# Kernel optimization log

Measured on AMD Instinct MI355X. Metric: run time of the kernel, lower is better.

The kernel has to match this reference:

```python
import jax, jax.numpy as jnp
import numpy as np

B, T, D, H, C = 64, 512, 128, 512, 256  # batch, seq_len, input_dim, rnn_dim, clf hidden


def _lstm_cell(x, h, c, Wih, Whh, b):
    # PyTorch gate order: i, f, g, o; b = bias_ih + bias_hh
    gates = x @ Wih.T + h @ Whh.T + b  # [B, 4H]
    i, f, g, o = jnp.split(gates, 4, axis=-1)
    c = jax.nn.sigmoid(f) * c + jax.nn.sigmoid(i) * jnp.tanh(g)
    h = jax.nn.sigmoid(o) * jnp.tanh(c)
    return h, c


def _run_lstm2(xs, state, p0, p1):
    # xs: [B, T, in]; state: (h0, c0, h1, c1) each [B, H]
    def step(carry, x_t):
        h0, c0, h1, c1 = carry
        h0, c0 = _lstm_cell(x_t, h0, c0, *p0)
        h1, c1 = _lstm_cell(h0, h1, c1, *p1)
        return (h0, c0, h1, c1), h1
    state, ys = jax.lax.scan(step, state, jnp.swapaxes(xs, 0, 1))
    return jnp.swapaxes(ys, 0, 1), state


def setup_inputs() -> dict:
    key = jax.random.key(0)
    ks = jax.random.split(key, 18)
    s = 0.04  # ~1/sqrt(H), matches torch LSTM init scale
    w = lambda k, shape: (jax.random.normal(k, shape, jnp.float32) * s)
    inp = {
        "x": jax.random.uniform(ks[0], (B, T, D), dtype=jnp.float32),
        "y": (jax.random.uniform(ks[1], (B, T, D), dtype=jnp.float32) > 0.9).astype(jnp.float32),
        "enc_Wih0": w(ks[2], (4 * H, D)), "enc_Whh0": w(ks[3], (4 * H, H)), "enc_b0": w(ks[4], (4 * H,)),
        "enc_Wih1": w(ks[5], (4 * H, H)), "enc_Whh1": w(ks[6], (4 * H, H)), "enc_b1": w(ks[7], (4 * H,)),
        "dec_Wih0": w(ks[8], (4 * H, D)), "dec_Whh0": w(ks[9], (4 * H, H)), "dec_b0": w(ks[10], (4 * H,)),
        "dec_Wih1": w(ks[11], (4 * H, H)), "dec_Whh1": w(ks[12], (4 * H, H)), "dec_b1": w(ks[13], (4 * H,)),
        "clf_W1": w(ks[14], (C, H)), "clf_b1": w(ks[15], (C,)),
        "clf_W2": w(ks[16], (D, C)), "clf_b2": w(ks[17], (D,)),
    }
    return inp


def reference(x, y, enc_Wih0, enc_Whh0, enc_b0, enc_Wih1, enc_Whh1, enc_b1,
              dec_Wih0, dec_Whh0, dec_b0, dec_Wih1, dec_Whh1, dec_b1,
              clf_W1, clf_b1, clf_W2, clf_b2):
    Bc = x.shape[0]
    z = jnp.zeros((Bc, H), x.dtype)
    # encoder: only final (h, c) of both layers is used
    _, state = _run_lstm2(x, (z, z, z, z),
                          (enc_Wih0, enc_Whh0, enc_b0), (enc_Wih1, enc_Whh1, enc_b1))
    # decoder under full teacher forcing: steps t=1..T-1 consume y[:, t-1]
    dec_out, _ = _run_lstm2(y[:, :-1], state,
                            (dec_Wih0, dec_Whh0, dec_b0), (dec_Wih1, dec_Whh1, dec_b1))
    hid = jax.nn.relu(dec_out @ clf_W1.T + clf_b1)          # [B, T-1, C]
    logits = hid @ clf_W2.T + clf_b2                        # [B, T-1, D]
    # outputs[:, 0] stays zero, as in the torch loop starting at t=1
    return jnp.concatenate([jnp.zeros_like(logits[:, :1]), logits], axis=1)
```

## Files before the change

### kernel.cpp

```cpp
#include <hip/hip_runtime.h>
#include <hip/hip_bf16.h>
#include <stdint.h>

#define SMEM_BYTES 150528

using short8  = __attribute__((ext_vector_type(8))) short;
using f32x4   = __attribute__((ext_vector_type(4))) float;
using u32x4   = __attribute__((ext_vector_type(4))) unsigned int;

#define OXBF 0u
#define OYBF 8388608u
#define OWE0 16777216u
#define OWD0 (OWE0 + 2621440u)
#define OWE1 (OWD0 + 2621440u)
#define OWD1 (OWE1 + 4194304u)
#define OWC1 (OWD1 + 4194304u)
#define OWC2 (OWC1 + 262144u)
#define OA0  (OWC2 + 65536u)
#define OB0  (OA0 + 2097152u)
#define OA1  (OB0 + 2097152u)
#define OB1  (OA1 + 2097152u)
#define OHP  (OB1 + 2097152u)
#define OFLG (OHP + 1048576u)
#define OFC1 (OFLG + 4096u)
#define OFH  (OFLG + 8192u)
#define OFL  (OFLG + 9216u)
#define OPRB (OFLG + 16384u)
#define OVOT (OFLG + 32768u)

#define GUARD (1<<19)

static __device__ __forceinline__ unsigned short f2bf(float f){
  union { float f; unsigned u; } v; v.f = f;
  unsigned r = v.u + 0x7FFFu + ((v.u >> 16) & 1u);
  return (unsigned short)(r >> 16);
}
static __device__ __forceinline__ float sigm(float x){ return 1.f/(1.f+__expf(-x)); }
static __device__ __forceinline__ float tanh_(float x){ return 1.f - 2.f/(__expf(2.f*x)+1.f); }

static __device__ __forceinline__ u32x4 ld_r16(const void* p, bool loc){
  u32x4 v;
  if (loc) asm volatile("global_load_dwordx4 %0, %1, off sc0"     : "=v"(v) : "v"(p) : "memory");
  else     asm volatile("global_load_dwordx4 %0, %1, off sc0 sc1" : "=v"(v) : "v"(p) : "memory");
  return v;
}
static __device__ __forceinline__ void st_r16(void* p, u32x4 v, bool loc){
  if (loc) asm volatile("global_store_dwordx4 %0, %1, off sc0"     :: "v"(p), "v"(v) : "memory");
  else     asm volatile("global_store_dwordx4 %0, %1, off sc0 sc1" :: "v"(p), "v"(v) : "memory");
}
static __device__ __forceinline__ unsigned ld_f4(const void* p, bool loc){
  unsigned v;
  if (loc) asm volatile("global_load_dword %0, %1, off sc0\n\ts_waitcnt vmcnt(0)"     : "=v"(v) : "v"(p) : "memory");
  else     asm volatile("global_load_dword %0, %1, off sc0 sc1\n\ts_waitcnt vmcnt(0)" : "=v"(v) : "v"(p) : "memory");
  return v;
}
static __device__ __forceinline__ void st_f4(void* p, unsigned v, bool loc){
  if (loc) asm volatile("global_store_dword %0, %1, off sc0"     :: "v"(p), "v"(v) : "memory");
  else     asm volatile("global_store_dword %0, %1, off sc0 sc1" :: "v"(p), "v"(v) : "memory");
}
static __device__ __forceinline__ unsigned ld_cg4(const void* p){ return ld_f4(p, false); }
static __device__ __forceinline__ void st_cg4(void* p, unsigned v){ st_f4(p, v, false); }
static __device__ __forceinline__ void drain_vm(){
  asm volatile("s_waitcnt vmcnt(0)" ::: "memory");
}
static __device__ __forceinline__ bool isS(u32x4 v){
  return (v[0]==0xFFFFFFFFu) | (v[1]==0xFFFFFFFFu) | (v[2]==0xFFFFFFFFu) | (v[3]==0xFFFFFFFFu);
}

__global__ void k_init(float* __restrict__ out, uint8_t* __restrict__ ws){
  int i = blockIdx.x*blockDim.x + threadIdx.x;
  int ns = gridDim.x*blockDim.x;
  uint32_t* r = (uint32_t*)(ws + OA0);
  const int nring = (4*2097152 + 1048576)/4;
  for (int k=i; k<nring; k+=ns) r[k] = 0xFFFFFFFFu;
  uint32_t* fl = (uint32_t*)(ws + OFLG);
  for (int k=i; k<49152/4; k+=ns) fl[k] = 0u;
  for (int k=i; k<64*128; k+=ns) out[(size_t)(k>>7)*(512*128) + (k&127)] = 0.f;
}

__global__ void k_cvt(const float* __restrict__ x, const float* __restrict__ y,
                      uint8_t* __restrict__ ws){
  unsigned short* xb = (unsigned short*)(ws + OXBF);
  unsigned short* yb = (unsigned short*)(ws + OYBF);
  const int n = 64*512*128;
  int i = blockIdx.x*blockDim.x + threadIdx.x, ns = gridDim.x*blockDim.x;
  for (int k=i; k<n; k+=ns){ xb[k] = f2bf(x[k]); yb[k] = f2bf(y[k]); }
}

__global__ void k_swzgate(const float* __restrict__ Wih, const float* __restrict__ Whh,
                          uint8_t* __restrict__ ws, size_t dstOff, int Kin, int KC, int NKK, int mode){
  unsigned short* dst = (unsigned short*)(ws + dstOff);
  const int total = 2048 * (KC*4);
  int i = blockIdx.x*blockDim.x + threadIdx.x, ns = gridDim.x*blockDim.x;
  for (int idx=i; idx<total; idx+=ns){
    int j = idx & 7;
    int lane = (idx >> 3) & 63;
    int t = idx >> 9;
    int g = t & 3; t >>= 2;
    int kk = t % NKK; t /= NKK;
    int w = t & 3; int ub = t >> 2;
    int off = ((lane>>4)<<3) + j;
    int k = mode ? (kk==0 ? w*32 + off : 128 + w*128 + (kk-1)*32 + off)
                 : (w*KC + kk*32 + off);
    int u = ub*16 + (lane&15);
    int row = g*512 + u;
    float v = (k < Kin) ? Wih[(size_t)row*Kin + k] : Whh[(size_t)row*512 + (k-Kin)];
    dst[idx] = f2bf(v);
  }
}

__global__ void k_swzclf(const float* __restrict__ W, uint8_t* __restrict__ ws,
                         size_t dstOff, int nwgs, int Kw, int Ktot){
  unsigned short* dst = (unsigned short*)(ws + dstOff);
  const int NKK = Kw/32;
  const int total = nwgs*4*NKK*64*8;
  int i = blockIdx.x*blockDim.x + threadIdx.x, ns = gridDim.x*blockDim.x;
  for (int idx=i; idx<total; idx+=ns){
    int j = idx & 7;
    int lane = (idx >> 3) & 63;
    int t = idx >> 9;
    int kk = t % NKK; t /= NKK;
    int w = t & 3; int wg = t >> 2;
    int k = w*Kw + kk*32 + ((lane>>4)<<3) + j;
    int col = wg*16 + (lane&15);
    dst[idx] = f2bf(W[(size_t)col*Ktot + k]);
  }
}

__launch_bounds__(256, 1)
__global__ void k_seq(uint8_t* __restrict__ ws,
                      const float* __restrict__ eb0, const float* __restrict__ eb1,
                      const float* __restrict__ db0, const float* __restrict__ db1,
                      const float* __restrict__ cb1, const float* __restrict__ cb2,
                      float* __restrict__ out){
  __shared__ uint8_t smem[SMEM_BYTES];
  const int wg = blockIdx.x, tid = threadIdx.x;
  const int w = tid>>6, l = tid&63, lr = l&15, lg = l>>4;
  const int xcd = wg & 7, j = wg >> 3;

  int role;
  if (xcd < 2) role = 0;
  else if (xcd < 4) role = 1;
  else if (xcd == 4 && j < 16) role = 2;
  else if (xcd == 4 && j < 24) role = 3;
  else return;

  const unsigned short* xb = (const unsigned short*)(ws+OXBF);
  const unsigned short* yb = (const unsigned short*)(ws+OYBF);
  unsigned short* A0e = (unsigned short*)(ws+OA0);
  unsigned short* B0e = (unsigned short*)(ws+OB0);
  unsigned short* A1e = (unsigned short*)(ws+OA1);
  unsigned short* B1e = (unsigned short*)(ws+OB1);
  unsigned short* hpr = (unsigned short*)(ws+OHP);

  short8* BL = (short8*)smem;
  float*  P0 = (float*)(smem + 131072);
  float*  P1 = (float*)(smem + 139776);
  unsigned short* HS = (unsigned short*)(smem + 148480);

  const u32x4 S4 = (u32x4){0xFFFFFFFFu,0xFFFFFFFFu,0xFFFFFFFFu,0xFFFFFFFFu};
  const u32x4 Z4 = (u32x4){0u,0u,0u,0u};

  bool loc;
  {
    const int n   = (role <= 1) ? 32 : 24;
    const int bas = (role <= 1) ? xcd : 4;
    if (w == 0){
      bool ok = true;
      #pragma unroll 1
      for (int gen = 1; gen <= 3; ++gen){
        if (l == 0) st_f4(ws + OPRB + (size_t)wg*64u, (unsigned)gen, true);
        if (l < n){
          const void* p = ws + OPRB + (size_t)(bas + 8*l)*64u;
          int spins = 0; unsigned e;
          do { e = ld_f4(p, true); } while ((int)e < gen && ++spins < 1024);
          if ((int)e < gen) ok = false;
        }
      }
      unsigned long long b1 = __ballot(ok);
      bool wgok = (b1 == ~0ULL);
      if (l == 0) st_f4(ws + OVOT + (size_t)wg*64u, wgok ? 2u : 1u, false);
      bool vok = wgok;
      if (l < n){
        const void* p = ws + OVOT + (size_t)(bas + 8*l)*64u;
        unsigned v;
        do { v = ld_f4(p, false); } while (v == 0u);
        vok = vok && (v == 2u);
      }
      unsigned long long b2 = __ballot(vok);
      if (l == 0) *(int*)HS = (b2 == ~0ULL) ? 1 : 0;
    }
    __syncthreads();
    loc = (*(volatile int*)HS) != 0;
    __syncthreads();
  }

  auto loadB = [&](size_t srcOff, int bytes){
    const u32x4* s = (const u32x4*)(ws + srcOff);
    u32x4* d = (u32x4*)smem;
    for (int i = tid; i < bytes/16; i += 256) d[i] = s[i];
  };

  if (role <= 1){
    const bool isC0 = (role == 0);
    const int bt = isC0 ? xcd : xcd-2, ub = j;
    const int u = tid&15, ug = ub*16 + u;
    const int bbytes = isC0 ? 81920 : 131072;
    unsigned short* OWN0 = loc ? A0e : B0e;

    float be[4], bd[4];
    {
      const float* e = isC0 ? eb0 : eb1;
      const float* d = isC0 ? db0 : db1;
      #pragma unroll
      for (int g=0; g<4; ++g){ be[g] = e[g*512+ug]; bd[g] = d[g*512+ug]; }
    }
    loadB((isC0 ? (size_t)OWE0 : (size_t)OWE1) + (size_t)ub*bbytes, bbytes);
    float cS0 = 0.f, cS1 = 0.f;
    __syncthreads();

    for (int t = 0; t < 1023; ++t){
      if (t == 512){
        __syncthreads();
        loadB((isC0 ? (size_t)OWD0 : (size_t)OWD1) + (size_t)ub*bbytes, bbytes);
        __syncthreads();
      }

      const int slotW = t&31, slotR = (t+31)&31;

      f32x4 acc[2][4];
      #pragma unroll
      for (int m=0;m<2;++m)
        #pragma unroll
        for (int g=0;g<4;++g) acc[m][g] = (f32x4){0.f,0.f,0.f,0.f};

      if (isC0){
        const unsigned short* xs = (t<512) ? xb : yb;
        const int tt = (t<512) ? t : t-512;
        short8 ax[2];
        #pragma unroll
        for (int m=0;m<2;++m){
          const int b = bt*32 + m*16 + lr;
          ax[m] = *(const short8*)(xs + ((size_t)b*512 + tt)*128 + w*32 + (lg<<3));
        }
        u32x4 ah[4][2];
        if (t > 0){
          const unsigned short* base = OWN0 + (size_t)slotR*64*512;
          int gd = 0; bool bad;
          do {
            #pragma unroll
            for (int kk=0; kk<4; ++kk)
              #pragma unroll
              for (int m=0;m<2;++m){
                const int b = bt*32 + m*16 + lr;
                ah[kk][m] = ld_r16(base + (size_t)b*512 + w*128 + kk*32 + (lg<<3), loc);
              }
            drain_vm();
            __builtin_amdgcn_sched_barrier(0);
            bad = false;
            #pragma unroll
            for (int kk=0; kk<4; ++kk)
              #pragma unroll
              for (int m=0;m<2;++m) bad |= isS(ah[kk][m]);
            if (bad) __builtin_amdgcn_s_sleep(1);
          } while (bad && ++gd < GUARD);
          __builtin_amdgcn_sched_barrier(0);
        } else {
          #pragma unroll
          for (int kk=0; kk<4; ++kk)
            #pragma unroll
            for (int m=0;m<2;++m) ah[kk][m] = Z4;
        }
        #pragma unroll
        for (int g=0;g<4;++g){
          short8 bf = BL[((w*5+0)*4+g)*64 + l];
          acc[0][g] = __builtin_amdgcn_mfma_f32_16x16x32_bf16(ax[0], bf, acc[0][g],0,0,0);
          acc[1][g] = __builtin_amdgcn_mfma_f32_16x16x32_bf16(ax[1], bf, acc[1][g],0,0,0);
        }
        #pragma unroll
        for (int kk=1; kk<5; ++kk)
          #pragma unroll
          for (int g=0;g<4;++g){
            short8 bf = BL[((w*5+kk)*4+g)*64 + l];
            acc[0][g] = __builtin_amdgcn_mfma_f32_16x16x32_bf16(__builtin_bit_cast(short8, ah[kk-1][0]), bf, acc[0][g],0,0,0);
            acc[1][g] = __builtin_amdgcn_mfma_f32_16x16x32_bf16(__builtin_bit_cast(short8, ah[kk-1][1]), bf, acc[1][g],0,0,0);
          }
      } else {
        u32x4 a[8][2];
        const bool wv01 = (w < 2);
        if (wv01 || t > 0){
          const unsigned short* base;
          bool myloc;
          if (wv01){ base = B0e + (size_t)slotW*64*512; myloc = false; }
          else {
            base = (loc ? A1e : (((t-1) >= 512) ? B1e : A1e)) + (size_t)slotR*64*512;
            myloc = loc;
          }
          const int kbase = wv01 ? (w*256) : (w*256 - 512);
          int gd = 0; bool bad;
          do {
            #pragma unroll
            for (int kk=0; kk<8; ++kk)
              #pragma unroll
              for (int m=0;m<2;++m){
                const int b = bt*32 + m*16 + lr;
                a[kk][m] = ld_r16(base + (size_t)b*512 + kbase + kk*32 + (lg<<3), myloc);
              }
            drain_vm();
            __builtin_amdgcn_sched_barrier(0);
            bad = false;
            #pragma unroll
            for (int kk=0; kk<8; ++kk)
              #pragma unroll
              for (int m=0;m<2;++m) bad |= isS(a[kk][m]);
            if (bad) __builtin_amdgcn_s_sleep(1);
          } while (bad && ++gd < GUARD);
          __builtin_amdgcn_sched_barrier(0);
        } else {
          #pragma unroll
          for (int kk=0; kk<8; ++kk)
            #pragma unroll
            for (int m=0;m<2;++m) a[kk][m] = Z4;
        }
        #pragma unroll
        for (int kk=0; kk<8; ++kk)
          #pragma unroll
          for (int g=0;g<4;++g){
            short8 bf = BL[((w*8+kk)*4+g)*64 + l];
            acc[0][g] = __builtin_amdgcn_mfma_f32_16x16x32_bf16(__builtin_bit_cast(short8, a[kk][0]), bf, acc[0][g],0,0,0);
            acc[1][g] = __builtin_amdgcn_mfma_f32_16x16x32_bf16(__builtin_bit_cast(short8, a[kk][1]), bf, acc[1][g],0,0,0);
          }
      }

      {
        float* P = (w&1) ? P1 : P0;
        if (w < 2){
          #pragma unroll
          for (int m=0;m<2;++m)
            #pragma unroll
            for (int g=0;g<4;++g)
              #pragma unroll
              for (int r=0;r<4;++r)
                P[(m*16 + (lg<<2) + r)*68 + g*16 + lr] = acc[m][g][r];
        }
        __syncthreads();
        if (w >= 2){
          #pragma unroll
          for (int m=0;m<2;++m)
            #pragma unroll
            for (int g=0;g<4;++g)
              #pragma unroll
              for (int r=0;r<4;++r)
                P[(m*16 + (lg<<2) + r)*68 + g*16 + lr] += acc[m][g][r];
        }
        __syncthreads();
      }

      if (w == 0 && (t & 7) == 0){
        drain_vm();
        __builtin_amdgcn_sched_barrier(0);
        if (isC0){
          if (t >= 24 && l < 32){
            const void* p = ws + OFC1 + (size_t)(bt*32+l)*64;
            const int need = (t-22 < 1) ? 1 : t-22;
            int v, gd = 0;
            do { v = (int)ld_f4(p, false); if (v < need) __builtin_amdgcn_s_sleep(2); }
            while (v < need && ++gd < GUARD);
          }
        } else {
          if (t >= 536 && l < 16){
            const void* p = ws + OFH + (size_t)l*64;
            const int need = (t-534 < 1) ? 1 : t-534;
            int v, gd = 0;
            do { v = (int)ld_f4(p, false); if (v < need) __builtin_amdgcn_s_sleep(2); }
            while (v < need && ++gd < GUARD);
          }
        }
        if (t >= 8){
          const int row = l>>1, half = l&1;
          #pragma unroll
          for (int a=2; a<=9; ++a){
            const int cs = (t+a)&31;
            const size_t off = ((size_t)cs*64 + bt*32 + row)*512 + ub*16 + half*8;
            if (isC0){
              st_r16(OWN0 + off, S4, loc);
              if (loc) st_r16(B0e + off, S4, false);
            } else {
              st_r16(loc ? A1e + off : (((t+a-32) >= 512) ? B1e + off : A1e + off), S4, loc ? true : false);
              if (loc && (t+a) >= 544) st_r16(B1e + off, S4, false);
            }
          }
        }
      }

      const float* bias = (t<512) ? be : bd;
      #pragma unroll
      for (int s=0;s<2;++s){
        const int row = (tid>>4) + s*16;
        const int pi = row*68 + u;
        float gi = P0[pi]      + P1[pi]      + bias[0];
        float gf = P0[pi+16]   + P1[pi+16]   + bias[1];
        float gg = P0[pi+32]   + P1[pi+32]   + bias[2];
        float go = P0[pi+48]   + P1[pi+48]   + bias[3];
        float cprev = s ? cS1 : cS0;
        float c = sigm(gf)*cprev + sigm(gi)*tanh_(gg);
        if (s) cS1 = c; else cS0 = c;
        float h = sigm(go)*tanh_(c);
        HS[row*16 + u] = f2bf(h);
      }
      __syncthreads();
      if (tid < 64){
        u32x4 v = *(const u32x4*)(HS + tid*8);
        const int row = tid>>1, half = tid&1;
        const size_t off = ((size_t)slotW*64 + bt*32 + row)*512 + ub*16 + half*8;
        if (isC0){
          st_r16(OWN0 + off, v, loc);
          if (loc) st_r16(B0e + off, v, false);
        } else {
          if (loc){
            st_r16(A1e + off, v, true);
            if (t >= 512) st_r16(B1e + off, v, false);
          } else {
            st_r16(((t >= 512) ? B1e : A1e) + off, v, false);
          }
        }
      }
      if (!isC0 && tid == 0)
        st_f4(ws + OFC1 + (size_t)(bt*32+ub)*64, (unsigned)(t+1), false);
    }
  } else if (role == 2){
    const int hwg = j;
    const int u = tid&15, col = hwg*16 + u;
    const float bc = cb1[col];
    loadB((size_t)OWC1 + (size_t)hwg*16384, 16384);
    __syncthreads();
    for (int t2 = 0; t2 < 511; ++t2){
      const int slot = (512+t2)&31;

      u32x4 a[4][4];
      const unsigned short* base = B1e + (size_t)slot*64*512;
      int gd = 0; bool bad;
      do {
        #pragma unroll
        for (int kk=0; kk<4; ++kk)
          #pragma unroll
          for (int m=0;m<4;++m)
            a[kk][m] = ld_r16(base + (size_t)(m*16+lr)*512 + w*128 + kk*32 + (lg<<3), false);
        drain_vm();
        __builtin_amdgcn_sched_barrier(0);
        bad = false;
        #pragma unroll
        for (int kk=0; kk<4; ++kk)
          #pragma unroll
          for (int m=0;m<4;++m) bad |= isS(a[kk][m]);
        if (bad) __builtin_amdgcn_s_sleep(1);
      } while (bad && ++gd < GUARD);
      __builtin_amdgcn_sched_barrier(0);
      f32x4 ha[4];
      #pragma unroll
      for (int m=0;m<4;++m) ha[m] = (f32x4){0.f,0.f,0.f,0.f};
      #pragma unroll
      for (int kk=0; kk<4; ++kk){
        short8 bf = BL[(w*4+kk)*64 + l];
        #pragma unroll
        for (int m=0;m<4;++m)
          ha[m] = __builtin_amdgcn_mfma_f32_16x16x32_bf16(__builtin_bit_cast(short8, a[kk][m]), bf, ha[m],0,0,0);
      }
      {
        float* P = (w&1) ? P1 : P0;
        if (w < 2){
          #pragma unroll
          for (int m=0;m<4;++m)
            #pragma unroll
            for (int r=0;r<4;++r)
              P[(m*16 + (lg<<2) + r)*20 + lr] = ha[m][r];
        }
        __syncthreads();
        if (w >= 2){
          #pragma unroll
          for (int m=0;m<4;++m)
            #pragma unroll
            for (int r=0;r<4;++r)
              P[(m*16 + (lg<<2) + r)*20 + lr] += ha[m][r];
        }
        __syncthreads();
      }
      if (w == 0 && (t2 & 7) == 0){
        drain_vm();
        __builtin_amdgcn_sched_barrier(0);
        if (t2 >= 24 && l < 8){
          const void* p = ws + OFL + (size_t)l*64;
          const int need = (t2-22 < 1) ? 1 : t2-22;
          int v, g2 = 0;
          do { v = (int)ld_f4(p, loc); if (v < need) __builtin_amdgcn_s_sleep(2); }
          while (v < need && ++g2 < GUARD);
        }
        if (t2 >= 8){
          #pragma unroll
          for (int a=2; a<=9; ++a){
            const int cs = (t2+a)&31;
            #pragma unroll
            for (int q=0;q<2;++q)
              st_r16(hpr + ((size_t)cs*64 + l)*256 + hwg*16 + q*8, S4, loc);
          }
        }
      }
      #pragma unroll
      for (int s=0;s<4;++s){
        const int row = (tid>>4) + s*16;
        float v = P0[row*20+u] + P1[row*20+u] + bc;
        HS[row*16 + u] = f2bf(fmaxf(v, 0.f));
      }
      __syncthreads();
      if (tid < 128){
        u32x4 v = *(const u32x4*)(HS + tid*8);
        const int row = tid>>1, half = tid&1;
        st_r16(hpr + ((size_t)(t2&31)*64 + row)*256 + hwg*16 + half*8, v, loc);
      }
      if (tid == 0) st_f4(ws + OFH + (size_t)hwg*64, (unsigned)(t2+1), false);
    }
  } else {
    const int lwg = j - 16;
    const int u = tid&15, col = lwg*16 + u;
    const float bc = cb2[col];
    loadB((size_t)OWC2 + (size_t)lwg*8192, 8192);
    __syncthreads();
    for (int t3 = 0; t3 < 511; ++t3){
      const int slot = t3&31;
      u32x4 a[2][4];
      const unsigned short* base = hpr + (size_t)slot*64*256;
      int gd = 0; bool bad;
      do {
        #pragma unroll
        for (int kk=0; kk<2; ++kk)
          #pragma unroll
          for (int m=0;m<4;++m)
            a[kk][m] = ld_r16(base + (size_t)(m*16+lr)*256 + w*64 + kk*32 + (lg<<3), loc);
        drain_vm();
        __builtin_amdgcn_sched_barrier(0);
        bad = false;
        #pragma unroll
        for (int kk=0; kk<2; ++kk)
          #pragma unroll
          for (int m=0;m<4;++m) bad |= isS(a[kk][m]);
        if (bad) __builtin_amdgcn_s_sleep(1);
      } while (bad && ++gd < GUARD);
      __builtin_amdgcn_sched_barrier(0);
      f32x4 la[4];
      #pragma unroll
      for (int m=0;m<4;++m) la[m] = (f32x4){0.f,0.f,0.f,0.f};
      #pragma unroll
      for (int kk=0; kk<2; ++kk){
        short8 bf = BL[(w*2+kk)*64 + l];
        #pragma unroll
        for (int m=0;m<4;++m)
          la[m] = __builtin_amdgcn_mfma_f32_16x16x32_bf16(__builtin_bit_cast(short8, a[kk][m]), bf, la[m],0,0,0);
      }
      {
        float* P = (w&1) ? P1 : P0;
        if (w < 2){
          #pragma unroll
          for (int m=0;m<4;++m)
            #pragma unroll
            for (int r=0;r<4;++r)
              P[(m*16 + (lg<<2) + r)*20 + lr] = la[m][r];
        }
        __syncthreads();
        if (w >= 2){
          #pragma unroll
          for (int m=0;m<4;++m)
            #pragma unroll
            for (int r=0;r<4;++r)
              P[(m*16 + (lg<<2) + r)*20 + lr] += la[m][r];
        }
        __syncthreads();
      }
      #pragma unroll
      for (int s=0;s<4;++s){
        const int row = (tid>>4) + s*16;
        float v = P0[row*20+u] + P1[row*20+u] + bc;
        out[((size_t)row*512 + (t3+1))*128 + col] = v;
      }
      if (tid == 0) st_f4(ws + OFL + (size_t)lwg*64, (unsigned)(t3+1), loc);
    }
  }
}

extern "C" void kernel_launch(void* const* d_in, const int* in_sizes, int n_in,
                              void* d_out, int out_size, void* d_ws, size_t ws_size,
                              hipStream_t stream){
  const float* x   = (const float*)d_in[0];
  const float* y   = (const float*)d_in[1];
  const float* eW0 = (const float*)d_in[2];
  const float* eU0 = (const float*)d_in[3];
  const float* eb0 = (const float*)d_in[4];
  const float* eW1 = (const float*)d_in[5];
  const float* eU1 = (const float*)d_in[6];
  const float* eb1 = (const float*)d_in[7];
  const float* dW0 = (const float*)d_in[8];
  const float* dU0 = (const float*)d_in[9];
  const float* db0 = (const float*)d_in[10];
  const float* dW1 = (const float*)d_in[11];
  const float* dU1 = (const float*)d_in[12];
  const float* db1 = (const float*)d_in[13];
  const float* cW1 = (const float*)d_in[14];
  const float* cb1 = (const float*)d_in[15];
  const float* cW2 = (const float*)d_in[16];
  const float* cb2 = (const float*)d_in[17];
  float* out = (float*)d_out;
  uint8_t* ws = (uint8_t*)d_ws;
  (void)in_sizes; (void)n_in; (void)out_size; (void)ws_size;

  k_init<<<dim3(256), dim3(256), 0, stream>>>(out, ws);
  k_cvt<<<dim3(2048), dim3(256), 0, stream>>>(x, y, ws);
  k_swzgate<<<dim3(1280), dim3(256), 0, stream>>>(eW0, eU0, ws, (size_t)OWE0, 128, 160, 5, 1);
  k_swzgate<<<dim3(1280), dim3(256), 0, stream>>>(dW0, dU0, ws, (size_t)OWD0, 128, 160, 5, 1);
  k_swzgate<<<dim3(2048), dim3(256), 0, stream>>>(eW1, eU1, ws, (size_t)OWE1, 512, 256, 8, 0);
  k_swzgate<<<dim3(2048), dim3(256), 0, stream>>>(dW1, dU1, ws, (size_t)OWD1, 512, 256, 8, 0);
  k_swzclf<<<dim3(256), dim3(256), 0, stream>>>(cW1, ws, (size_t)OWC1, 16, 128, 512);
  k_swzclf<<<dim3(64),  dim3(256), 0, stream>>>(cW2, ws, (size_t)OWC2, 8, 64, 256);
  k_seq<<<dim3(256), dim3(256), 0, stream>>>(ws, eb0, eb1, db0, db1, cb1, cb2, out);
}
```

Baseline: 5.209 ms.

## Add dedicated comm wave and replace block barriers with LDS flag handshakes

Adds a fifth wavefront per workgroup that handles the global h-ring publish, slot poisoning and cross-workgroup flag polling. The four compute waves now coordinate through LDS counters with spin-waits instead of __syncthreads, and the h staging buffer is double-buffered so the next step's compute can overlap the previous step's publish. This aims to take global-store latency and periodic poll stalls off the recurrent critical path. In exchange it adds spin-wait overhead and more complex ordering, with a risk of races or hangs if the fences are wrong.

```diff
diff --git a/kernel.cpp b/kernel.cpp
--- a/kernel.cpp
+++ b/kernel.cpp
@@ -2,7 +2,7 @@
 #include <hip/hip_bf16.h>
 #include <stdint.h>
 
-#define SMEM_BYTES 150528
+#define SMEM_BYTES 152640
 
 using short8  = __attribute__((ext_vector_type(8))) short;
 using f32x4   = __attribute__((ext_vector_type(4))) float;
@@ -58,10 +58,11 @@
   if (loc) asm volatile("global_store_dword %0, %1, off sc0"     :: "v"(p), "v"(v) : "memory");
   else     asm volatile("global_store_dword %0, %1, off sc0 sc1" :: "v"(p), "v"(v) : "memory");
 }
-static __device__ __forceinline__ unsigned ld_cg4(const void* p){ return ld_f4(p, false); }
-static __device__ __forceinline__ void st_cg4(void* p, unsigned v){ st_f4(p, v, false); }
 static __device__ __forceinline__ void drain_vm(){
   asm volatile("s_waitcnt vmcnt(0)" ::: "memory");
+}
+static __device__ __forceinline__ void drain_lgkm(){
+  asm volatile("s_waitcnt lgkmcnt(0)" ::: "memory");
 }
 static __device__ __forceinline__ bool isS(u32x4 v){
   return (v[0]==0xFFFFFFFFu) | (v[1]==0xFFFFFFFFu) | (v[2]==0xFFFFFFFFu) | (v[3]==0xFFFFFFFFu);
@@ -127,7 +128,7 @@
   }
 }
 
-__launch_bounds__(256, 1)
+__launch_bounds__(320, 1)
 __global__ void k_seq(uint8_t* __restrict__ ws,
                       const float* __restrict__ eb0, const float* __restrict__ eb1,
                       const float* __restrict__ db0, const float* __restrict__ db1,
@@ -157,6 +158,10 @@
   float*  P0 = (float*)(smem + 131072);
   float*  P1 = (float*)(smem + 139776);
   unsigned short* HS = (unsigned short*)(smem + 148480);
+  volatile int* FL  = (volatile int*)(smem + 152576);
+  volatile int* DBE = (volatile int*)(smem + 152592);
+  volatile int* DBC = (volatile int*)(smem + 152608);
+  volatile int* FW  = (volatile int*)(smem + 152612);
 
   const u32x4 S4 = (u32x4){0xFFFFFFFFu,0xFFFFFFFFu,0xFFFFFFFFu,0xFFFFFFFFu};
   const u32x4 Z4 = (u32x4){0u,0u,0u,0u};
@@ -194,11 +199,24 @@
     loc = (*(volatile int*)HS) != 0;
     __syncthreads();
   }
+  if (tid < 16) ((volatile int*)(smem + 152576))[tid] = 0;
+  __syncthreads();
 
   auto loadB = [&](size_t srcOff, int bytes){
-    const u32x4* s = (const u32x4*)(ws + srcOff);
-    u32x4* d = (u32x4*)smem;
-    for (int i = tid; i < bytes/16; i += 256) d[i] = s[i];
+    if (tid < 256){
+      const u32x4* s = (const u32x4*)(ws + srcOff);
+      u32x4* d = (u32x4*)smem;
+      for (int i = tid; i < bytes/16; i += 256) d[i] = s[i];
+    }
+  };
+  auto spin_ge = [&](volatile int* p, int tgt){
+    int g = 0;
+    while (*p < tgt && ++g < GUARD) __builtin_amdgcn_s_sleep(1);
+    __builtin_amdgcn_sched_barrier(0);
+  };
+  auto set_fl = [&](volatile int* p, int v){
+    drain_lgkm();
+    if (l == 0) *p = v;
   };
 
   if (role <= 1){
@@ -219,122 +237,127 @@
     float cS0 = 0.f, cS1 = 0.f;
     __syncthreads();
 
-    for (int t = 0; t < 1023; ++t){
-      if (t == 512){
-        __syncthreads();
-        loadB((isC0 ? (size_t)OWD0 : (size_t)OWD1) + (size_t)ub*bbytes, bbytes);
-        __syncthreads();
-      }
-
-      const int slotW = t&31, slotR = (t+31)&31;
-
-      f32x4 acc[2][4];
-      #pragma unroll
-      for (int m=0;m<2;++m)
-        #pragma unroll
-        for (int g=0;g<4;++g) acc[m][g] = (f32x4){0.f,0.f,0.f,0.f};
-
-      if (isC0){
-        const unsigned short* xs = (t<512) ? xb : yb;
-        const int tt = (t<512) ? t : t-512;
-        short8 ax[2];
-        #pragma unroll
-        for (int m=0;m<2;++m){
-          const int b = bt*32 + m*16 + lr;
-          ax[m] = *(const short8*)(xs + ((size_t)b*512 + tt)*128 + w*32 + (lg<<3));
-        }
-        u32x4 ah[4][2];
-        if (t > 0){
-          const unsigned short* base = OWN0 + (size_t)slotR*64*512;
-          int gd = 0; bool bad;
-          do {
+    if (w < 4){
+      for (int t = 0; t < 1023; ++t){
+        if (t == 512){
+          #pragma unroll 1
+          for (int q=0;q<4;++q) spin_ge(&DBE[q], 512);
+          loadB((isC0 ? (size_t)OWD0 : (size_t)OWD1) + (size_t)ub*bbytes, bbytes);
+          drain_vm(); drain_lgkm();
+          set_fl(&FW[w], 1);
+          #pragma unroll 1
+          for (int q=0;q<4;++q) spin_ge(&FW[q], 1);
+        }
+        const int slotW = t&31, slotR = (t+31)&31;
+
+        f32x4 acc[2][4];
+        #pragma unroll
+        for (int m=0;m<2;++m)
+          #pragma unroll
+          for (int g=0;g<4;++g) acc[m][g] = (f32x4){0.f,0.f,0.f,0.f};
+
+        if (isC0){
+          const unsigned short* xs = (t<512) ? xb : yb;
+          const int tt = (t<512) ? t : t-512;
+          short8 ax[2];
+          #pragma unroll
+          for (int m=0;m<2;++m){
+            const int b = bt*32 + m*16 + lr;
+            ax[m] = *(const short8*)(xs + ((size_t)b*512 + tt)*128 + w*32 + (lg<<3));
+          }
+          u32x4 ah[4][2];
+          if (t > 0){
+            const unsigned short* base = OWN0 + (size_t)slotR*64*512;
+            int gd = 0; bool bad;
+            do {
+              #pragma unroll
+              for (int kk=0; kk<4; ++kk)
+                #pragma unroll
+                for (int m=0;m<2;++m){
+                  const int b = bt*32 + m*16 + lr;
+                  ah[kk][m] = ld_r16(base + (size_t)b*512 + w*128 + kk*32 + (lg<<3), loc);
+                }
+              drain_vm();
+              __builtin_amdgcn_sched_barrier(0);
+              bad = false;
+              #pragma unroll
+              for (int kk=0; kk<4; ++kk)
+                #pragma unroll
+                for (int m=0;m<2;++m) bad |= isS(ah[kk][m]);
+              if (bad) __builtin_amdgcn_s_sleep(1);
+            } while (bad && ++gd < GUARD);
+            __builtin_amdgcn_sched_barrier(0);
+          } else {
             #pragma unroll
             for (int kk=0; kk<4; ++kk)
               #pragma unroll
-              for (int m=0;m<2;++m){
-                const int b = bt*32 + m*16 + lr;
-                ah[kk][m] = ld_r16(base + (size_t)b*512 + w*128 + kk*32 + (lg<<3), loc);
-              }
-            drain_vm();
+              for (int m=0;m<2;++m) ah[kk][m] = Z4;
+          }
+          #pragma unroll
+          for (int g=0;g<4;++g){
+            short8 bf = BL[((w*5+0)*4+g)*64 + l];
+            acc[0][g] = __builtin_amdgcn_mfma_f32_16x16x32_bf16(ax[0], bf, acc[0][g],0,0,0);
+            acc[1][g] = __builtin_amdgcn_mfma_f32_16x16x32_bf16(ax[1], bf, acc[1][g],0,0,0);
+          }
+          #pragma unroll
+          for (int kk=1; kk<5; ++kk)
+            #pragma unroll
+            for (int g=0;g<4;++g){
+              short8 bf = BL[((w*5+kk)*4+g)*64 + l];
+              acc[0][g] = __builtin_amdgcn_mfma_f32_16x16x32_bf16(__builtin_bit_cast(short8, ah[kk-1][0]), bf, acc[0][g],0,0,0);
+              acc[1][g] = __builtin_amdgcn_mfma_f32_16x16x32_bf16(__builtin_bit_cast(short8, ah[kk-1][1]), bf, acc[1][g],0,0,0);
+            }
+        } else {
+          u32x4 a[8][2];
+          const bool wv01 = (w < 2);
+          if (wv01 || t > 0){
+            const unsigned short* base;
+            bool myloc;
+            if (wv01){ base = B0e + (size_t)slotW*64*512; myloc = false; }
+            else {
+              base = (loc ? A1e : (((t-1) >= 512) ? B1e : A1e)) + (size_t)slotR*64*512;
+              myloc = loc;
+            }
+            const int kbase = wv01 ? (w*256) : (w*256 - 512);
+            int gd = 0; bool bad;
+            do {
+              #pragma unroll
+              for (int kk=0; kk<8; ++kk)
+                #pragma unroll
+                for (int m=0;m<2;++m){
+                  const int b = bt*32 + m*16 + lr;
+                  a[kk][m] = ld_r16(base + (size_t)b*512 + kbase + kk*32 + (lg<<3), myloc);
+                }
+              drain_vm();
+              __builtin_amdgcn_sched_barrier(0);
+              bad = false;
+              #pragma unroll
+              for (int kk=0; kk<8; ++kk)
+                #pragma unroll
+                for (int m=0;m<2;++m) bad |= isS(a[kk][m]);
+              if (bad) __builtin_amdgcn_s_sleep(1);
+            } while (bad && ++gd < GUARD);
             __builtin_amdgcn_sched_barrier(0);
-            bad = false;
-            #pragma unroll
-            for (int kk=0; kk<4; ++kk)
-              #pragma unroll
-              for (int m=0;m<2;++m) bad |= isS(ah[kk][m]);
-            if (bad) __builtin_amdgcn_s_sleep(1);
-          } while (bad && ++gd < GUARD);
-          __builtin_amdgcn_sched_barrier(0);
-        } else {
-          #pragma unroll
-          for (int kk=0; kk<4; ++kk)
-            #pragma unroll
-            for (int m=0;m<2;++m) ah[kk][m] = Z4;
-        }
-        #pragma unroll
-        for (int g=0;g<4;++g){
-          short8 bf = BL[((w*5+0)*4+g)*64 + l];
-          acc[0][g] = __builtin_amdgcn_mfma_f32_16x16x32_bf16(ax[0], bf, acc[0][g],0,0,0);
-          acc[1][g] = __builtin_amdgcn_mfma_f32_16x16x32_bf16(ax[1], bf, acc[1][g],0,0,0);
-        }
-        #pragma unroll
-        for (int kk=1; kk<5; ++kk)
-          #pragma unroll
-          for (int g=0;g<4;++g){
-            short8 bf = BL[((w*5+kk)*4+g)*64 + l];
-            acc[0][g] = __builtin_amdgcn_mfma_f32_16x16x32_bf16(__builtin_bit_cast(short8, ah[kk-1][0]), bf, acc[0][g],0,0,0);
-            acc[1][g] = __builtin_amdgcn_mfma_f32_16x16x32_bf16(__builtin_bit_cast(short8, ah[kk-1][1]), bf, acc[1][g],0,0,0);
-          }
-      } else {
-        u32x4 a[8][2];
-        const bool wv01 = (w < 2);
-        if (wv01 || t > 0){
-          const unsigned short* base;
-          bool myloc;
-          if (wv01){ base = B0e + (size_t)slotW*64*512; myloc = false; }
-          else {
-            base = (loc ? A1e : (((t-1) >= 512) ? B1e : A1e)) + (size_t)slotR*64*512;
-            myloc = loc;
-          }
-          const int kbase = wv01 ? (w*256) : (w*256 - 512);
-          int gd = 0; bool bad;
-          do {
+          } else {
             #pragma unroll
             for (int kk=0; kk<8; ++kk)
               #pragma unroll
-              for (int m=0;m<2;++m){
-                const int b = bt*32 + m*16 + lr;
-                a[kk][m] = ld_r16(base + (size_t)b*512 + kbase + kk*32 + (lg<<3), myloc);
-              }
-            drain_vm();
-            __builtin_amdgcn_sched_barrier(0);
-            bad = false;
-            #pragma unroll
-            for (int kk=0; kk<8; ++kk)
-              #pragma unroll
-              for (int m=0;m<2;++m) bad |= isS(a[kk][m]);
-            if (bad) __builtin_amdgcn_s_sleep(1);
-          } while (bad && ++gd < GUARD);
-          __builtin_amdgcn_sched_barrier(0);
-        } else {
+              for (int m=0;m<2;++m) a[kk][m] = Z4;
+          }
           #pragma unroll
           for (int kk=0; kk<8; ++kk)
             #pragma unroll
-            for (int m=0;m<2;++m) a[kk][m] = Z4;
-        }
-        #pragma unroll
-        for (int kk=0; kk<8; ++kk)
-          #pragma unroll
-          for (int g=0;g<4;++g){
-            short8 bf = BL[((w*8+kk)*4+g)*64 + l];
-            acc[0][g] = __builtin_amdgcn_mfma_f32_16x16x32_bf16(__builtin_bit_cast(short8, a[kk][0]), bf, acc[0][g],0,0,0);
-            acc[1][g] = __builtin_amdgcn_mfma_f32_16x16x32_bf16(__builtin_bit_cast(short8, a[kk][1]), bf, acc[1][g],0,0,0);
-          }
-      }
-
-      {
-        float* P = (w&1) ? P1 : P0;
+            for (int g=0;g<4;++g){
+              short8 bf = BL[((w*8+kk)*4+g)*64 + l];
+              acc[0][g] = __builtin_amdgcn_mfma_f32_16x16x32_bf16(__builtin_bit_cast(short8, a[kk][0]), bf, acc[0][g],0,0,0);
+              acc[1][g] = __builtin_amdgcn_mfma_f32_16x16x32_bf16(__builtin_bit_cast(short8, a[kk][1]), bf, acc[1][g],0,0,0);
+            }
+        }
+
         if (w < 2){
+          #pragma unroll 1
+          for (int q=0;q<4;++q) spin_ge(&DBE[q], t);
+          float* P = (w&1) ? P1 : P0;
           #pragma unroll
           for (int m=0;m<2;++m)
             #pragma unroll
@@ -342,9 +365,10 @@
               #pragma unroll
               for (int r=0;r<4;++r)
                 P[(m*16 + (lg<<2) + r)*68 + g*16 + lr] = acc[m][g][r];
-        }
-        __syncthreads();
-        if (w >= 2){
+          set_fl(&FL[w], t+1);
+        } else {
+          spin_ge(&FL[w-2], t+1);
+          float* P = (w&1) ? P1 : P0;
           #pragma unroll
           for (int m=0;m<2;++m)
             #pragma unroll
@@ -352,67 +376,73 @@
               #pragma unroll
               for (int r=0;r<4;++r)
                 P[(m*16 + (lg<<2) + r)*68 + g*16 + lr] += acc[m][g][r];
-        }
-        __syncthreads();
-      }
-
-      if (w == 0 && (t & 7) == 0){
-        drain_vm();
-        __builtin_amdgcn_sched_barrier(0);
-        if (isC0){
-          if (t >= 24 && l < 32){
-            const void* p = ws + OFC1 + (size_t)(bt*32+l)*64;
-            const int need = (t-22 < 1) ? 1 : t-22;
-            int v, gd = 0;
-            do { v = (int)ld_f4(p, false); if (v < need) __builtin_amdgcn_s_sleep(2); }
-            while (v < need && ++gd < GUARD);
-          }
-        } else {
-          if (t >= 536 && l < 16){
-            const void* p = ws + OFH + (size_t)l*64;
-            const int need = (t-534 < 1) ? 1 : t-534;
-            int v, gd = 0;
-            do { v = (int)ld_f4(p, false); if (v < need) __builtin_amdgcn_s_sleep(2); }
-            while (v < need && ++gd < GUARD);
-          }
-        }
-        if (t >= 8){
-          const int row = l>>1, half = l&1;
-          #pragma unroll
-          for (int a=2; a<=9; ++a){
-            const int cs = (t+a)&31;
-            const size_t off = ((size_t)cs*64 + bt*32 + row)*512 + ub*16 + half*8;
-            if (isC0){
-              st_r16(OWN0 + off, S4, loc);
-              if (loc) st_r16(B0e + off, S4, false);
-            } else {
-              st_r16(loc ? A1e + off : (((t+a-32) >= 512) ? B1e + off : A1e + off), S4, loc ? true : false);
-              if (loc && (t+a) >= 544) st_r16(B1e + off, S4, false);
+          set_fl(&FL[w], t+1);
+        }
+        spin_ge(&FL[2], t+1);
+        spin_ge(&FL[3], t+1);
+
+        const float* bias = (t<512) ? be : bd;
+        spin_ge(&DBC[0], t-1);
+        unsigned short* HSb = HS + (t&1)*512;
+        #pragma unroll
+        for (int s=0;s<2;++s){
+          const int row = (tid>>4) + s*16;
+          const int pi = row*68 + u;
+          float gi = P0[pi]      + P1[pi]      + bias[0];
+          float gf = P0[pi+16]   + P1[pi+16]   + bias[1];
+          float gg = P0[pi+32]   + P1[pi+32]   + bias[2];
+          float go = P0[pi+48]   + P1[pi+48]   + bias[3];
+          float cprev = s ? cS1 : cS0;
+          float c = sigm(gf)*cprev + sigm(gi)*tanh_(gg);
+          if (s) cS1 = c; else cS0 = c;
+          float h = sigm(go)*tanh_(c);
+          HSb[row*16 + u] = f2bf(h);
+        }
+        set_fl(&DBE[w], t+1);
+      }
+    } else {
+      for (int t = 0; t < 1023; ++t){
+        #pragma unroll 1
+        for (int q=0;q<4;++q) spin_ge(&DBE[q], t+1);
+        if ((t & 7) == 0){
+          drain_vm();
+          __builtin_amdgcn_sched_barrier(0);
+          if (isC0){
+            if (t >= 24 && l < 32){
+              const void* p = ws + OFC1 + (size_t)(bt*32+l)*64;
+              const int need = (t-22 < 1) ? 1 : t-22;
+              int v, gd = 0;
+              do { v = (int)ld_f4(p, false); if (v < need) __builtin_amdgcn_s_sleep(2); }
+              while (v < need && ++gd < GUARD);
             }
-          }
-        }
-      }
-
-      const float* bias = (t<512) ? be : bd;
-      #pragma unroll
-      for (int s=0;s<2;++s){
-        const int row = (tid>>4) + s*16;
-        const int pi = row*68 + u;
-        float gi = P0[pi]      + P1[pi]      + bias[0];
-        float gf = P0[pi+16]   + P1[pi+16]   + bias[1];
-        float gg = P0[pi+32]   + P1[pi+32]   + bias[2];
-        float go = P0[pi+48]   + P1[pi+48]   + bias[3];
-        float cprev = s ? cS1 : cS0;
-        float c = sigm(gf)*cprev + sigm(gi)*tanh_(gg);
-        if (s) cS1 = c; else cS0 = c;
-        float h = sigm(go)*tanh_(c);
-        HS[row*16 + u] = f2bf(h);
-      }
-      __syncthreads();
-      if (tid < 64){
-        u32x4 v = *(const u32x4*)(HS + tid*8);
-        const int row = tid>>1, half = tid&1;
-        const size_t off = ((size_t)slotW*64 + bt*32 + row)*512 + ub*16 + half*8;
+          } else {
+            if (t >= 536 && l < 16){
+              const void* p = ws + OFH + (size_t)l*64;
+              const int need = (t-534 < 1) ? 1 : t-534;
+              int v, gd = 0;
+              do { v = (int)ld_f4(p, false); if (v < need) __builtin_amdgcn_s_sleep(2); }
+              while (v < need && ++gd < GUARD);
+            }
+          }
+          if (t >= 8){
+            const int row = l>>1, half = l&1;
+            #pragma unroll
+            for (int a=2; a<=9; ++a){
+              const int cs = (t+a)&31;
+              const size_t off = ((size_t)cs*64 + bt*32 + row)*512 + ub*16 + half*8;
+              if (isC0){
+                st_r16(OWN0 + off, S4, loc);
+                if (loc) st_r16(B0e + off, S4, false);
+              } else {
+                st_r16(loc ? A1e + off : (((t+a-32) >= 512) ? B1e + off : A1e + off), S4, loc ? true : false);
+                if (loc && (t+a) >= 544) st_r16(B1e + off, S4, false);
+              }
+            }
+          }
+        }
+        u32x4 v = *(const u32x4*)(HS + (t&1)*512 + l*8);
+        const int row = l>>1, half = l&1;
+        const size_t off = ((size_t)(t&31)*64 + bt*32 + row)*512 + ub*16 + half*8;
         if (isC0){
           st_r16(OWN0 + off, v, loc);
           if (loc) st_r16(B0e + off, v, false);
@@ -424,9 +454,11 @@
             st_r16(((t >= 512) ? B1e : A1e) + off, v, false);
           }
         }
-      }
-      if (!isC0 && tid == 0)
-        st_f4(ws + OFC1 + (size_t)(bt*32+ub)*64, (unsigned)(t+1), false);
+        if (!isC0 && l == 0)
+          st_f4(ws + OFC1 + (size_t)(bt*32+ub)*64, (unsigned)(t+1), false);
+        drain_lgkm();
+        if (l == 0) DBC[0] = t+1;
+      }
     }
   } else if (role == 2){
     const int hwg = j;
@@ -434,90 +466,106 @@
     const float bc = cb1[col];
     loadB((size_t)OWC1 + (size_t)hwg*16384, 16384);
     __syncthreads();
-    for (int t2 = 0; t2 < 511; ++t2){
-      const int slot = (512+t2)&31;
-
-      u32x4 a[4][4];
-      const unsigned short* base = B1e + (size_t)slot*64*512;
-      int gd = 0; bool bad;
-      do {
-        #pragma unroll
-        for (int kk=0; kk<4; ++kk)
+
+    if (w < 4){
+      for (int t2 = 0; t2 < 511; ++t2){
+        const int slot = (512+t2)&31;
+        u32x4 a[4][4];
+        const unsigned short* base = B1e + (size_t)slot*64*512;
+        int gd = 0; bool bad;
+        do {
+          #pragma unroll
+          for (int kk=0; kk<4; ++kk)
+            #pragma unroll
+            for (int m=0;m<4;++m)
+              a[kk][m] = ld_r16(base + (size_t)(m*16+lr)*512 + w*128 + kk*32 + (lg<<3), false);
+          drain_vm();
+          __builtin_amdgcn_sched_barrier(0);
+          bad = false;
+          #pragma unroll
+          for (int kk=0; kk<4; ++kk)
+            #pragma unroll
+            for (int m=0;m<4;++m) bad |= isS(a[kk][m]);
+          if (bad) __builtin_amdgcn_s_sleep(1);
+        } while (bad && ++gd < GUARD);
+        __builtin_amdgcn_sched_barrier(0);
+        f32x4 ha[4];
+        #pragma unroll
+        for (int m=0;m<4;++m) ha[m] = (f32x4){0.f,0.f,0.f,0.f};
+        #pragma unroll
+        for (int kk=0; kk<4; ++kk){
+          short8 bf = BL[(w*4+kk)*64 + l];
           #pragma unroll
           for (int m=0;m<4;++m)
-            a[kk][m] = ld_r16(base + (size_t)(m*16+lr)*512 + w*128 + kk*32 + (lg<<3), false);
-        drain_vm();
-        __builtin_amdgcn_sched_barrier(0);
-        bad = false;
-        #pragma unroll
-        for (int kk=0; kk<4; ++kk)
-          #pragma unroll
-          for (int m=0;m<4;++m) bad |= isS(a[kk][m]);
-        if (bad) __builtin_amdgcn_s_sleep(1);
-      } while (bad && ++gd < GUARD);
-      __builtin_amdgcn_sched_barrier(0);
-      f32x4 ha[4];
-      #pragma unroll
-      for (int m=0;m<4;++m) ha[m] = (f32x4){0.f,0.f,0.f,0.f};
-      #pragma unroll
-      for (int kk=0; kk<4; ++kk){
-        short8 bf = BL[(w*4+kk)*64 + l];
-        #pragma unroll
-        for (int m=0;m<4;++m)
-          ha[m] = __builtin_amdgcn_mfma_f32_16x16x32_bf16(__builtin_bit_cast(short8, a[kk][m]), bf, ha[m],0,0,0);
-      }
-      {
-        float* P = (w&1) ? P1 : P0;
+            ha[m] = __builtin_amdgcn_mfma_f32_16x16x32_bf16(__builtin_bit_cast(short8, a[kk][m]), bf, ha[m],0,0,0);
+        }
         if (w < 2){
+          #pragma unroll 1
+          for (int q=0;q<4;++q) spin_ge(&DBE[q], t2);
+          float* P = (w&1) ? P1 : P0;
           #pragma unroll
           for (int m=0;m<4;++m)
             #pragma unroll
             for (int r=0;r<4;++r)
               P[(m*16 + (lg<<2) + r)*20 + lr] = ha[m][r];
-        }
-        __syncthreads();
-        if (w >= 2){
+          set_fl(&FL[w], t2+1);
+        } else {
+          spin_ge(&FL[w-2], t2+1);
+          float* P = (w&1) ? P1 : P0;
           #pragma unroll
           for (int m=0;m<4;++m)
             #pragma unroll
             for (int r=0;r<4;++r)
               P[(m*16 + (lg<<2) + r)*20 + lr] += ha[m][r];
-        }
-        __syncthreads();
-      }
-      if (w == 0 && (t2 & 7) == 0){
-        drain_vm();
-        __builtin_amdgcn_sched_barrier(0);
-        if (t2 >= 24 && l < 8){
-          const void* p = ws + OFL + (size_t)l*64;
-          const int need = (t2-22 < 1) ? 1 : t2-22;
-          int v, g2 = 0;
-          do { v = (int)ld_f4(p, loc); if (v < need) __builtin_amdgcn_s_sleep(2); }
-          while (v < need && ++g2 < GUARD);
-        }
-        if (t2 >= 8){
-          #pragma unroll
-          for (int a=2; a<=9; ++a){
-            const int cs = (t2+a)&31;
-            #pragma unroll
-            for (int q=0;q<2;++q)
-              st_r16(hpr + ((size_t)cs*64 + l)*256 + hwg*16 + q*8, S4, loc);
-          }
-        }
-      }
-      #pragma unroll
-      for (int s=0;s<4;++s){
-        const int row = (tid>>4) + s*16;
-        float v = P0[row*20+u] + P1[row*20+u] + bc;
-        HS[row*16 + u] = f2bf(fmaxf(v, 0.f));
-      }
-      __syncthreads();
-      if (tid < 128){
-        u32x4 v = *(const u32x4*)(HS + tid*8);
-        const int row = tid>>1, half = tid&1;
-        st_r16(hpr + ((size_t)(t2&31)*64 + row)*256 + hwg*16 + half*8, v, loc);
-      }
-      if (tid == 0) st_f4(ws + OFH + (size_t)hwg*64, (unsigned)(t2+1), false);
+          set_fl(&FL[w], t2+1);
+        }
+        spin_ge(&FL[2], t2+1);
+        spin_ge(&FL[3], t2+1);
+        spin_ge(&DBC[0], t2-1);
+        unsigned short* HSb = HS + (t2&1)*1024;
+        #pragma unroll
+        for (int s=0;s<4;++s){
+          const int row = (tid>>4) + s*16;
+          float v = P0[row*20+u] + P1[row*20+u] + bc;
+          HSb[row*16 + u] = f2bf(fmaxf(v, 0.f));
+        }
+        set_fl(&DBE[w], t2+1);
+      }
+    } else {
+      for (int t2 = 0; t2 < 511; ++t2){
+        #pragma unroll 1
+        for (int q=0;q<4;++q) spin_ge(&DBE[q], t2+1);
+        if ((t2 & 7) == 0){
+          drain_vm();
+          __builtin_amdgcn_sched_barrier(0);
+          if (t2 >= 24 && l < 8){
+            const void* p = ws + OFL + (size_t)l*64;
+            const int need = (t2-22 < 1) ? 1 : t2-22;
+            int v, g2 = 0;
+            do { v = (int)ld_f4(p, loc); if (v < need) __builtin_amdgcn_s_sleep(2); }
+            while (v < need && ++g2 < GUARD);
+          }
+          if (t2 >= 8){
+            #pragma unroll
+            for (int a=2; a<=9; ++a){
+              const int cs = (t2+a)&31;
+              #pragma unroll
+              for (int q=0;q<2;++q)
+                st_r16(hpr + ((size_t)cs*64 + l)*256 + hwg*16 + q*8, S4, loc);
+            }
+          }
+        }
+        #pragma unroll
+        for (int q=0;q<2;++q){
+          const int i = l + q*64;
+          u32x4 v = *(const u32x4*)(HS + (t2&1)*1024 + i*8);
+          const int row = i>>1, half = i&1;
+          st_r16(hpr + ((size_t)(t2&31)*64 + row)*256 + hwg*16 + half*8, v, loc);
+        }
+        if (l == 0) st_f4(ws + OFH + (size_t)hwg*64, (unsigned)(t2+1), false);
+        drain_lgkm();
+        if (l == 0) DBC[0] = t2+1;
+      }
     }
   } else {
     const int lwg = j - 16;
@@ -525,63 +573,75 @@
     const float bc = cb2[col];
     loadB((size_t)OWC2 + (size_t)lwg*8192, 8192);
     __syncthreads();
-    for (int t3 = 0; t3 < 511; ++t3){
-      const int slot = t3&31;
-      u32x4 a[2][4];
-      const unsigned short* base = hpr + (size_t)slot*64*256;
-      int gd = 0; bool bad;
-      do {
-        #pragma unroll
-        for (int kk=0; kk<2; ++kk)
+
+    if (w < 4){
+      for (int t3 = 0; t3 < 511; ++t3){
+        const int slot = t3&31;
+        u32x4 a[2][4];
+        const unsigned short* base = hpr + (size_t)slot*64*256;
+        int gd = 0; bool bad;
+        do {
+          #pragma unroll
+          for (int kk=0; kk<2; ++kk)
+            #pragma unroll
+            for (int m=0;m<4;++m)
+              a[kk][m] = ld_r16(base + (size_t)(m*16+lr)*256 + w*64 + kk*32 + (lg<<3), loc);
+          drain_vm();
+          __builtin_amdgcn_sched_barrier(0);
+          bad = false;
+          #pragma unroll
+          for (int kk=0; kk<2; ++kk)
+            #pragma unroll
+            for (int m=0;m<4;++m) bad |= isS(a[kk][m]);
+          if (bad) __builtin_amdgcn_s_sleep(1);
+        } while (bad && ++gd < GUARD);
+        __builtin_amdgcn_sched_barrier(0);
+        f32x4 la[4];
+        #pragma unroll
+        for (int m=0;m<4;++m) la[m] = (f32x4){0.f,0.f,0.f,0.f};
+        #pragma unroll
+        for (int kk=0; kk<2; ++kk){
+          short8 bf = BL[(w*2+kk)*64 + l];
           #pragma unroll
           for (int m=0;m<4;++m)
-            a[kk][m] = ld_r16(base + (size_t)(m*16+lr)*256 + w*64 + kk*32 + (lg<<3), loc);
-        drain_vm();
-        __builtin_amdgcn_sched_barrier(0);
-        bad = false;
-        #pragma unroll
-        for (int kk=0; kk<2; ++kk)
-          #pragma unroll
-          for (int m=0;m<4;++m) bad |= isS(a[kk][m]);
-        if (bad) __builtin_amdgcn_s_sleep(1);
-      } while (bad && ++gd < GUARD);
-      __builtin_amdgcn_sched_barrier(0);
-      f32x4 la[4];
-      #pragma unroll
-      for (int m=0;m<4;++m) la[m] = (f32x4){0.f,0.f,0.f,0.f};
-      #pragma unroll
-      for (int kk=0; kk<2; ++kk){
-        short8 bf = BL[(w*2+kk)*64 + l];
-        #pragma unroll
-        for (int m=0;m<4;++m)
-          la[m] = __builtin_amdgcn_mfma_f32_16x16x32_bf16(__builtin_bit_cast(short8, a[kk][m]), bf, la[m],0,0,0);
-      }
-      {
-        float* P = (w&1) ? P1 : P0;
+            la[m] = __builtin_amdgcn_mfma_f32_16x16x32_bf16(__builtin_bit_cast(short8, a[kk][m]), bf, la[m],0,0,0);
+        }
         if (w < 2){
+          #pragma unroll 1
+          for (int q=0;q<4;++q) spin_ge(&DBE[q], t3);
+          float* P = (w&1) ? P1 : P0;
           #pragma unroll
           for (int m=0;m<4;++m)
             #pragma unroll
             for (int r=0;r<4;++r)
               P[(m*16 + (lg<<2) + r)*20 + lr] = la[m][r];
-        }
-        __syncthreads();
-        if (w >= 2){
+          set_fl(&FL[w], t3+1);
+        } else {
+          spin_ge(&FL[w-2], t3+1);
+          float* P = (w&1) ? P1 : P0;
           #pragma unroll
           for (int m=0;m<4;++m)
             #pragma unroll
             for (int r=0;r<4;++r)
               P[(m*16 + (lg<<2) + r)*20 + lr] += la[m][r];
-        }
-        __syncthreads();
-      }
-      #pragma unroll
-      for (int s=0;s<4;++s){
-        const int row = (tid>>4) + s*16;
-        float v = P0[row*20+u] + P1[row*20+u] + bc;
-        out[((size_t)row*512 + (t3+1))*128 + col] = v;
-      }
-      if (tid == 0) st_f4(ws + OFL + (size_t)lwg*64, (unsigned)(t3+1), loc);
+          set_fl(&FL[w], t3+1);
+        }
+        spin_ge(&FL[2], t3+1);
+        spin_ge(&FL[3], t3+1);
+        #pragma unroll
+        for (int s=0;s<4;++s){
+          const int row = (tid>>4) + s*16;
+          float v = P0[row*20+u] + P1[row*20+u] + bc;
+          out[((size_t)row*512 + (t3+1))*128 + col] = v;
+        }
+        set_fl(&DBE[w], t3+1);
+      }
+    } else {
+      for (int t3 = 0; t3 < 511; ++t3){
+        #pragma unroll 1
+        for (int q=0;q<4;++q) spin_ge(&DBE[q], t3+1);
+        if (l == 0) st_f4(ws + OFL + (size_t)lwg*64, (unsigned)(t3+1), loc);
+      }
     }
   }
 }
@@ -619,5 +679,5 @@
   k_swzgate<<<dim3(2048), dim3(256), 0, stream>>>(dW1, dU1, ws, (size_t)OWD1, 512, 256, 8, 0);
   k_swzclf<<<dim3(256), dim3(256), 0, stream>>>(cW1, ws, (size_t)OWC1, 16, 128, 512);
   k_swzclf<<<dim3(64),  dim3(256), 0, stream>>>(cW2, ws, (size_t)OWC2, 8, 64, 256);
-  k_seq<<<dim3(256), dim3(256), 0, stream>>>(ws, eb0, eb1, db0, db1, cb1, cb2, out);
-}
+  k_seq<<<dim3(256), dim3(320), 0, stream>>>(ws, eb0, eb1, db0, db1, cb1, cb2, out);
+}
```

Measured after the change: 9.587 ms. 1.84x slower.
